# Performance work log

Measured on AMD Instinct MI355X. Metric: run time of the kernel, lower is better.

Reference implementation:

```python
import jax, jax.numpy as jnp
import numpy as np

NUM_HEADS = 12
WINDOW = (14, 14)


def gen_relative_position_index(ws):
    num_rel = (2 * ws[0] - 1) * (2 * ws[1] - 1) + 3
    coords = np.stack(np.meshgrid(np.arange(ws[0]), np.arange(ws[1]), indexing='ij'))
    cf = coords.reshape(2, -1)  # [2, Wh*Ww]
    rel = cf[:, :, None] - cf[:, None, :]  # [2, A, A]
    rel = rel.transpose(1, 2, 0).astype(np.int64)  # [A, A, 2]
    rel[..., 0] += ws[0] - 1
    rel[..., 1] += ws[1] - 1
    rel[..., 0] *= 2 * ws[1] - 1
    area = ws[0] * ws[1]
    idx = np.zeros((area + 1, area + 1), dtype=np.int64)
    idx[1:, 1:] = rel.sum(-1)
    idx[0, :] = num_rel - 3
    idx[:, 0] = num_rel - 2
    idx[0, 0] = num_rel - 1
    return idx


def setup_inputs() -> dict:
    key = jax.random.key(0)
    ks = jax.random.split(key, 7)
    B, N, C = 128, WINDOW[0] * WINDOW[1] + 1, 768
    num_rel = (2 * WINDOW[0] - 1) * (2 * WINDOW[1] - 1) + 3  # 732
    s = 0.02
    return {
        'x': jax.random.normal(ks[0], (B, N, C), jnp.float32),
        'qkv_w': jax.random.normal(ks[1], (3 * C, C), jnp.float32) * s,
        'q_bias': jax.random.normal(ks[2], (C,), jnp.float32) * s,
        'v_bias': jax.random.normal(ks[3], (C,), jnp.float32) * s,
        'rel_pos_table': jax.random.normal(ks[4], (num_rel, NUM_HEADS), jnp.float32) * s,
        'proj_w': jax.random.normal(ks[5], (C, C), jnp.float32) * s,
        'proj_b': jax.random.normal(ks[6], (C,), jnp.float32) * s,
        'rel_index': jnp.asarray(gen_relative_position_index(WINDOW)),
    }


def reference(x, qkv_w, q_bias, v_bias, rel_pos_table, proj_w, proj_b, rel_index):
    B, N, C = x.shape
    H = NUM_HEADS
    hd = C // H
    scale = hd ** -0.5
    # qkv projection with (q_bias, zeros, v_bias) composite bias
    bias = jnp.concatenate([q_bias, jnp.zeros_like(q_bias), v_bias])
    qkv = x @ qkv_w.T + bias  # [B, N, 3C]
    qkv = qkv.reshape(B, N, 3, H, hd).transpose(2, 0, 3, 1, 4)  # [3, B, H, N, hd]
    q, k, v = qkv[0], qkv[1], qkv[2]
    # gather relative position bias: [N, N, H] -> [H, N, N]
    rel_bias = rel_pos_table[rel_index.reshape(-1)].reshape(N, N, H).transpose(2, 0, 1)
    attn = jnp.einsum('bhnd,bhmd->bhnm', q * scale, k) + rel_bias[None]
    attn = jax.nn.softmax(attn, axis=-1)
    out = jnp.einsum('bhnm,bhmd->bhnd', attn, v)  # [B, H, N, hd]
    out = out.transpose(0, 2, 1, 3).reshape(B, N, C)
    return out @ proj_w.T + proj_b
```

## Files before the change

### kernel.cpp

```cpp
#include <hip/hip_runtime.h>

typedef unsigned short u16;
typedef __attribute__((ext_vector_type(8))) short short8;
typedef __attribute__((ext_vector_type(8))) __bf16 bf16x8;
typedef __attribute__((ext_vector_type(4))) float floatx4;

#define BATCH 128
#define SEQ 197
#define CH 768
#define NH 12
#define HD 64
#define MROWS (BATCH * SEQ)

__device__ __forceinline__ floatx4 mfma16(short8 a, short8 b, floatx4 c) {
  return __builtin_amdgcn_mfma_f32_16x16x32_bf16(
      __builtin_bit_cast(bf16x8, a), __builtin_bit_cast(bf16x8, b), c, 0, 0, 0);
}

__device__ __forceinline__ u16 f2bf(float f) {
  unsigned u = __builtin_bit_cast(unsigned, f);
  return (u16)((u + 0x7fffu + ((u >> 16) & 1u)) >> 16);
}

__device__ __forceinline__ void async16(const u16* g, u16* s) {
  __builtin_amdgcn_global_load_lds((const __attribute__((address_space(1))) void*)g,
                                   (__attribute__((address_space(3))) void*)s, 16, 0, 0);
}

__global__ __launch_bounds__(256) void preproc(const float4* __restrict__ x, ushort4* __restrict__ xo, int n0,
                                               const float4* __restrict__ w1, ushort4* __restrict__ w1o, int n1,
                                               const float4* __restrict__ w2, ushort4* __restrict__ w2o, int n2,
                                               const int* __restrict__ idx, const float* __restrict__ table,
                                               float* __restrict__ relb) {
  int i = blockIdx.x * 256 + threadIdx.x;
  const float4* in; ushort4* out; int j;
  if (i < n0) { in = x; out = xo; j = i; }
  else if (i < n0 + n1) { in = w1; out = w1o; j = i - n0; }
  else if (i < n0 + n1 + n2) { in = w2; out = w2o; j = i - n0 - n1; }
  else {
    int t = i - (n0 + n1 + n2);
    if (t < SEQ * SEQ) {
      int id = idx[t];
      const float* row = table + id * NH;
#pragma unroll
      for (int h = 0; h < NH; h++) relb[h * (SEQ * SEQ) + t] = row[h];
    }
    return;
  }
  float4 v = in[j];
  ushort4 o;
  o.x = f2bf(v.x); o.y = f2bf(v.y); o.z = f2bf(v.z); o.w = f2bf(v.w);
  out[j] = o;
}

__global__ __launch_bounds__(256, 2) void gemm_qkv(const u16* __restrict__ A,
                                                   const u16* __restrict__ W,
                                                   const float* __restrict__ qb,
                                                   const float* __restrict__ vb,
                                                   u16* __restrict__ q_buf,
                                                   u16* __restrict__ k_buf,
                                                   u16* __restrict__ v_buf) {
  __shared__ u16 As[128 * 32];
  __shared__ u16 Bs[256 * 32];
  int tid = threadIdx.x;
  int wave = tid >> 6, lane = tid & 63, quad = lane >> 4, c16 = lane & 15;
  int wm = wave >> 1, wn = wave & 1;
  int m0 = blockIdx.y * 128, n0 = blockIdx.x * 256;
  int lrow = lane >> 2;
  int lcol = (((lane & 3) ^ ((lane >> 3) & 3))) * 8;
  const u16* Ag0 = A + (size_t)(m0 + wave * 32 + lrow) * CH + lcol;
  const u16* Ag1 = Ag0 + (size_t)16 * CH;
  const u16* Bg0 = W + (size_t)(n0 + wave * 64 + lrow) * CH + lcol;
  const u16* Bg1 = Bg0 + (size_t)16 * CH;
  const u16* Bg2 = Bg0 + (size_t)32 * CH;
  const u16* Bg3 = Bg0 + (size_t)48 * CH;
  u16* AsW0 = As + (wave * 32) * 32;
  u16* AsW1 = As + (wave * 32 + 16) * 32;
  u16* BsW0 = Bs + (wave * 64) * 32;
  u16* BsW1 = Bs + (wave * 64 + 16) * 32;
  u16* BsW2 = Bs + (wave * 64 + 32) * 32;
  u16* BsW3 = Bs + (wave * 64 + 48) * 32;
  int fsl = (quad ^ ((c16 >> 1) & 3)) * 8;
  const u16* ArF = As + (wm * 64 + c16) * 32 + fsl;
  const u16* BrF = Bs + (wn * 128 + c16) * 32 + fsl;
  floatx4 acc[4][8] = {};
  for (int kk = 0; kk < CH; kk += 32) {
    __syncthreads();
    async16(Ag0 + kk, AsW0);
    async16(Ag1 + kk, AsW1);
    async16(Bg0 + kk, BsW0);
    async16(Bg1 + kk, BsW1);
    async16(Bg2 + kk, BsW2);
    async16(Bg3 + kk, BsW3);
    __syncthreads();
    short8 af[4], bfr[8];
#pragma unroll
    for (int i = 0; i < 4; i++) af[i] = *(const short8*)(ArF + i * 16 * 32);
#pragma unroll
    for (int j = 0; j < 8; j++) bfr[j] = *(const short8*)(BrF + j * 16 * 32);
#pragma unroll
    for (int i = 0; i < 4; i++)
#pragma unroll
      for (int j = 0; j < 8; j++) acc[i][j] = mfma16(af[i], bfr[j], acc[i][j]);
  }
#pragma unroll
  for (int j = 0; j < 8; j++) {
    int gcol = n0 + wn * 128 + j * 16 + c16;
    int t = gcol / CH;
    int rem = gcol - t * CH;
    int h = rem >> 6, d = rem & 63;
    float badd = (t == 0) ? qb[rem] : (t == 2 ? vb[rem] : 0.0f);
    u16* dst = (t == 0) ? q_buf : (t == 1 ? k_buf : v_buf);
#pragma unroll
    for (int i = 0; i < 4; i++) {
#pragma unroll
      for (int r = 0; r < 4; r++) {
        int grow = m0 + wm * 64 + i * 16 + quad * 4 + r;
        int bb = grow / SEQ;
        int n = grow - bb * SEQ;
        dst[(((size_t)bb * NH + h) * SEQ + n) * HD + d] = f2bf(acc[i][j][r] + badd);
      }
    }
  }
}

#define PS 232
#define VS 264

__global__ __launch_bounds__(256, 2) void attn(const u16* __restrict__ q_buf,
                                               const u16* __restrict__ k_buf,
                                               const u16* __restrict__ v_buf,
                                               const float* __restrict__ relb,
                                               u16* __restrict__ attn_out) {
  __shared__ u16 Vt[64 * VS];
  __shared__ u16 P[4 * 16 * PS];

  int h = blockIdx.x, b = blockIdx.y;
  int tid = threadIdx.x, wave = tid >> 6, lane = tid & 63, quad = lane >> 4, c16 = lane & 15;
  size_t bh = (size_t)b * NH + h;
  const u16* Q = q_buf + bh * SEQ * HD;
  const u16* Kp = k_buf + bh * SEQ * HD;
  const u16* Vp = v_buf + bh * SEQ * HD;
  const float* RB = relb + (size_t)h * (SEQ * SEQ);

  {
    int mrow = tid >> 3, dbase = (tid & 7) * 8;
#pragma unroll
    for (int i = 0; i < 7; i++) {
      int m = mrow + 32 * i;
      if (m < SEQ) {
        ushort4 v0 = *(const ushort4*)(Vp + m * HD + dbase);
        ushort4 v1 = *(const ushort4*)(Vp + m * HD + dbase + 4);
        Vt[(dbase + 0) * VS + m] = v0.x;
        Vt[(dbase + 1) * VS + m] = v0.y;
        Vt[(dbase + 2) * VS + m] = v0.z;
        Vt[(dbase + 3) * VS + m] = v0.w;
        Vt[(dbase + 4) * VS + m] = v1.x;
        Vt[(dbase + 5) * VS + m] = v1.y;
        Vt[(dbase + 6) * VS + m] = v1.z;
        Vt[(dbase + 7) * VS + m] = v1.w;
      } else {
#pragma unroll
        for (int dd = 0; dd < 8; dd++) Vt[(dbase + dd) * VS + m] = 0;
      }
    }
  }
  __syncthreads();

  u16* Pw = P + wave * 16 * PS;
  for (int rt = wave; rt < 13; rt += 4) {
    int q0 = rt * 16;
    int qr = min(q0 + c16, SEQ - 1);
    short8 qa0 = *(const short8*)(Q + qr * HD + quad * 8);
    short8 qa1 = *(const short8*)(Q + qr * HD + 32 + quad * 8);

    floatx4 sacc[13];
#pragma unroll
    for (int nt = 0; nt < 13; nt++) {
      int mc = min(nt * 16 + c16, SEQ - 1);
      floatx4 a = {0.f, 0.f, 0.f, 0.f};
      a = mfma16(qa0, *(const short8*)(Kp + mc * HD + quad * 8), a);
      a = mfma16(qa1, *(const short8*)(Kp + mc * HD + 32 + quad * 8), a);
      sacc[nt] = a;
    }

#pragma unroll
    for (int r = 0; r < 4; r++) {
      int rq = min(q0 + quad * 4 + r, SEQ - 1);
      const float* RBr = RB + (size_t)rq * SEQ;
      float mx = -1e30f;
#pragma unroll
      for (int nt = 0; nt < 13; nt++) {
        int m = nt * 16 + c16;
        float s = -1e30f;
        if (m < SEQ) s = sacc[nt][r] * 0.125f + RBr[m];
        sacc[nt][r] = s;
        mx = fmaxf(mx, s);
      }
      mx = fmaxf(mx, __shfl_xor(mx, 1));
      mx = fmaxf(mx, __shfl_xor(mx, 2));
      mx = fmaxf(mx, __shfl_xor(mx, 4));
      mx = fmaxf(mx, __shfl_xor(mx, 8));
      float sum = 0.f;
#pragma unroll
      for (int nt = 0; nt < 13; nt++) {
        float e = __expf(sacc[nt][r] - mx);
        sacc[nt][r] = e;
        sum += e;
      }
      sum += __shfl_xor(sum, 1);
      sum += __shfl_xor(sum, 2);
      sum += __shfl_xor(sum, 4);
      sum += __shfl_xor(sum, 8);
      float inv = 1.f / sum;
      int prow = (quad * 4 + r) * PS;
#pragma unroll
      for (int nt = 0; nt < 13; nt++)
        Pw[prow + nt * 16 + c16] = f2bf(sacc[nt][r] * inv);
      Pw[prow + 208 + c16] = 0;
    }

    floatx4 oacc[4] = {};
#pragma unroll
    for (int ks = 0; ks < 7; ks++) {
      short8 a = *(const short8*)(Pw + c16 * PS + ks * 32 + quad * 8);
#pragma unroll
      for (int dt = 0; dt < 4; dt++) {
        short8 bb = *(const short8*)(Vt + (dt * 16 + c16) * VS + ks * 32 + quad * 8);
        oacc[dt] = mfma16(a, bb, oacc[dt]);
      }
    }
#pragma unroll
    for (int dt = 0; dt < 4; dt++) {
      int d = dt * 16 + c16;
#pragma unroll
      for (int r = 0; r < 4; r++) {
        int grow = q0 + quad * 4 + r;
        if (grow < SEQ)
          attn_out[((size_t)b * SEQ + grow) * CH + h * HD + d] = f2bf(oacc[dt][r]);
      }
    }
  }
}

__global__ __launch_bounds__(256, 2) void gemm_proj(const u16* __restrict__ A,
                                                    const u16* __restrict__ W,
                                                    const float* __restrict__ bias,
                                                    float* __restrict__ out) {
  __shared__ u16 As[128 * 32];
  __shared__ u16 Bs[256 * 32];
  int tid = threadIdx.x;
  int wave = tid >> 6, lane = tid & 63, quad = lane >> 4, c16 = lane & 15;
  int wm = wave >> 1, wn = wave & 1;
  int m0 = blockIdx.y * 128, n0 = blockIdx.x * 256;
  int lrow = lane >> 2;
  int lcol = (((lane & 3) ^ ((lane >> 3) & 3))) * 8;
  const u16* Ag0 = A + (size_t)(m0 + wave * 32 + lrow) * CH + lcol;
  const u16* Ag1 = Ag0 + (size_t)16 * CH;
  const u16* Bg0 = W + (size_t)(n0 + wave * 64 + lrow) * CH + lcol;
  const u16* Bg1 = Bg0 + (size_t)16 * CH;
  const u16* Bg2 = Bg0 + (size_t)32 * CH;
  const u16* Bg3 = Bg0 + (size_t)48 * CH;
  u16* AsW0 = As + (wave * 32) * 32;
  u16* AsW1 = As + (wave * 32 + 16) * 32;
  u16* BsW0 = Bs + (wave * 64) * 32;
  u16* BsW1 = Bs + (wave * 64 + 16) * 32;
  u16* BsW2 = Bs + (wave * 64 + 32) * 32;
  u16* BsW3 = Bs + (wave * 64 + 48) * 32;
  int fsl = (quad ^ ((c16 >> 1) & 3)) * 8;
  const u16* ArF = As + (wm * 64 + c16) * 32 + fsl;
  const u16* BrF = Bs + (wn * 128 + c16) * 32 + fsl;
  floatx4 acc[4][8] = {};
  for (int kk = 0; kk < CH; kk += 32) {
    __syncthreads();
    async16(Ag0 + kk, AsW0);
    async16(Ag1 + kk, AsW1);
    async16(Bg0 + kk, BsW0);
    async16(Bg1 + kk, BsW1);
    async16(Bg2 + kk, BsW2);
    async16(Bg3 + kk, BsW3);
    __syncthreads();
    short8 af[4], bfr[8];
#pragma unroll
    for (int i = 0; i < 4; i++) af[i] = *(const short8*)(ArF + i * 16 * 32);
#pragma unroll
    for (int j = 0; j < 8; j++) bfr[j] = *(const short8*)(BrF + j * 16 * 32);
#pragma unroll
    for (int i = 0; i < 4; i++)
#pragma unroll
      for (int j = 0; j < 8; j++) acc[i][j] = mfma16(af[i], bfr[j], acc[i][j]);
  }
#pragma unroll
  for (int j = 0; j < 8; j++) {
    int gcol = n0 + wn * 128 + j * 16 + c16;
    float bj = bias[gcol];
#pragma unroll
    for (int i = 0; i < 4; i++)
#pragma unroll
      for (int r = 0; r < 4; r++) {
        int grow = m0 + wm * 64 + i * 16 + quad * 4 + r;
        out[(size_t)grow * CH + gcol] = acc[i][j][r] + bj;
      }
  }
}

extern "C" void kernel_launch(void* const* d_in, const int* in_sizes, int n_in,
                              void* d_out, int out_size, void* d_ws, size_t ws_size,
                              hipStream_t stream) {
  const float* x      = (const float*)d_in[0];
  const float* qkv_w  = (const float*)d_in[1];
  const float* q_bias = (const float*)d_in[2];
  const float* v_bias = (const float*)d_in[3];
  const float* table  = (const float*)d_in[4];
  const float* proj_w = (const float*)d_in[5];
  const float* proj_b = (const float*)d_in[6];
  const int*   rel_ix = (const int*)d_in[7];
  float* out = (float*)d_out;

  char* ws = (char*)d_ws;
  size_t off = 0;
  u16* x_bf  = (u16*)(ws + off); off += (size_t)MROWS * CH * 2;
  u16* wq_bf = (u16*)(ws + off); off += (size_t)3 * CH * CH * 2;
  u16* wp_bf = (u16*)(ws + off); off += (size_t)CH * CH * 2;
  u16* q_buf = (u16*)(ws + off); off += (size_t)MROWS * CH * 2;
  u16* k_buf = (u16*)(ws + off); off += (size_t)MROWS * CH * 2;
  u16* v_buf = (u16*)(ws + off); off += (size_t)MROWS * CH * 2;
  u16* ao_bf = (u16*)(ws + off); off += (size_t)MROWS * CH * 2;
  float* relb = (float*)(ws + off);

  int n0 = MROWS * CH / 4;
  int n1 = 3 * CH * CH / 4;
  int n2 = CH * CH / 4;
  int ntot = n0 + n1 + n2 + SEQ * SEQ;
  preproc<<<(ntot + 255) / 256, 256, 0, stream>>>(
      (const float4*)x, (ushort4*)x_bf, n0,
      (const float4*)qkv_w, (ushort4*)wq_bf, n1,
      (const float4*)proj_w, (ushort4*)wp_bf, n2,
      rel_ix, table, relb);
  gemm_qkv<<<dim3(9, 197), 256, 0, stream>>>(x_bf, wq_bf, q_bias, v_bias, q_buf, k_buf, v_buf);
  attn<<<dim3(NH, BATCH), 256, 0, stream>>>(q_buf, k_buf, v_buf, relb, ao_bf);
  gemm_proj<<<dim3(3, 197), 256, 0, stream>>>(ao_bf, wp_bf, proj_b, out);
}
```

Before: 419.7 us.

## Double-buffer LDS in QKV and proj GEMMs and remap blocks per XCD

Result: faster. 402.6 us (-4.1%).

```diff
diff --git a/kernel.cpp b/kernel.cpp
--- a/kernel.cpp
+++ b/kernel.cpp
@@ -60,12 +60,21 @@
                                                    u16* __restrict__ q_buf,
                                                    u16* __restrict__ k_buf,
                                                    u16* __restrict__ v_buf) {
-  __shared__ u16 As[128 * 32];
-  __shared__ u16 Bs[256 * 32];
+  __shared__ u16 S[2][(128 + 256) * 32];
+  const int BUF = (128 + 256) * 32;
+  const int BOFF = 128 * 32;
   int tid = threadIdx.x;
   int wave = tid >> 6, lane = tid & 63, quad = lane >> 4, c16 = lane & 15;
   int wm = wave >> 1, wn = wave & 1;
-  int m0 = blockIdx.y * 128, n0 = blockIdx.x * 256;
+
+  int nwg = gridDim.x;
+  int orig = blockIdx.x;
+  int xcd = orig & 7, pos = orig >> 3;
+  int qq = nwg >> 3, rr = nwg & 7;
+  int lid = (xcd < rr ? xcd * (qq + 1) : rr * (qq + 1) + (xcd - rr) * qq) + pos;
+  int mblk = lid / 9, nblk = lid - mblk * 9;
+  int m0 = mblk * 128, n0 = nblk * 256;
+
   int lrow = lane >> 2;
   int lcol = (((lane & 3) ^ ((lane >> 3) & 3))) * 8;
   const u16* Ag0 = A + (size_t)(m0 + wave * 32 + lrow) * CH + lcol;
@@ -74,35 +83,67 @@
   const u16* Bg1 = Bg0 + (size_t)16 * CH;
   const u16* Bg2 = Bg0 + (size_t)32 * CH;
   const u16* Bg3 = Bg0 + (size_t)48 * CH;
-  u16* AsW0 = As + (wave * 32) * 32;
-  u16* AsW1 = As + (wave * 32 + 16) * 32;
-  u16* BsW0 = Bs + (wave * 64) * 32;
-  u16* BsW1 = Bs + (wave * 64 + 16) * 32;
-  u16* BsW2 = Bs + (wave * 64 + 32) * 32;
-  u16* BsW3 = Bs + (wave * 64 + 48) * 32;
+  int aw0 = (wave * 32) * 32;
+  int aw1 = (wave * 32 + 16) * 32;
+  int bw0 = BOFF + (wave * 64) * 32;
+  int bw1 = BOFF + (wave * 64 + 16) * 32;
+  int bw2 = BOFF + (wave * 64 + 32) * 32;
+  int bw3 = BOFF + (wave * 64 + 48) * 32;
   int fsl = (quad ^ ((c16 >> 1) & 3)) * 8;
-  const u16* ArF = As + (wm * 64 + c16) * 32 + fsl;
-  const u16* BrF = Bs + (wn * 128 + c16) * 32 + fsl;
+  int aro = (wm * 64 + c16) * 32 + fsl;
+  int bro = BOFF + (wn * 128 + c16) * 32 + fsl;
+
   floatx4 acc[4][8] = {};
-  for (int kk = 0; kk < CH; kk += 32) {
-    __syncthreads();
-    async16(Ag0 + kk, AsW0);
-    async16(Ag1 + kk, AsW1);
-    async16(Bg0 + kk, BsW0);
-    async16(Bg1 + kk, BsW1);
-    async16(Bg2 + kk, BsW2);
-    async16(Bg3 + kk, BsW3);
-    __syncthreads();
+  u16* sbase = &S[0][0];
+
+  async16(Ag0, sbase + aw0);
+  async16(Ag1, sbase + aw1);
+  async16(Bg0, sbase + bw0);
+  async16(Bg1, sbase + bw1);
+  async16(Bg2, sbase + bw2);
+  async16(Bg3, sbase + bw3);
+  asm volatile("s_waitcnt vmcnt(0)" ::: "memory");
+  __builtin_amdgcn_s_barrier();
+  asm volatile("" ::: "memory");
+
+  int cur = 0;
+  for (int kt = 1; kt < CH / 32; ++kt) {
+    int kk = kt * 32;
+    u16* sn = sbase + (cur ^ 1) * BUF;
+    async16(Ag0 + kk, sn + aw0);
+    async16(Ag1 + kk, sn + aw1);
+    async16(Bg0 + kk, sn + bw0);
+    async16(Bg1 + kk, sn + bw1);
+    async16(Bg2 + kk, sn + bw2);
+    async16(Bg3 + kk, sn + bw3);
+    const u16* sc = sbase + cur * BUF;
     short8 af[4], bfr[8];
 #pragma unroll
-    for (int i = 0; i < 4; i++) af[i] = *(const short8*)(ArF + i * 16 * 32);
-#pragma unroll
-    for (int j = 0; j < 8; j++) bfr[j] = *(const short8*)(BrF + j * 16 * 32);
+    for (int i = 0; i < 4; i++) af[i] = *(const short8*)(sc + aro + i * 16 * 32);
+#pragma unroll
+    for (int j = 0; j < 8; j++) bfr[j] = *(const short8*)(sc + bro + j * 16 * 32);
 #pragma unroll
     for (int i = 0; i < 4; i++)
 #pragma unroll
       for (int j = 0; j < 8; j++) acc[i][j] = mfma16(af[i], bfr[j], acc[i][j]);
-  }
+    asm volatile("s_waitcnt vmcnt(0)" ::: "memory");
+    __builtin_amdgcn_s_barrier();
+    asm volatile("" ::: "memory");
+    cur ^= 1;
+  }
+  {
+    const u16* sc = sbase + cur * BUF;
+    short8 af[4], bfr[8];
+#pragma unroll
+    for (int i = 0; i < 4; i++) af[i] = *(const short8*)(sc + aro + i * 16 * 32);
+#pragma unroll
+    for (int j = 0; j < 8; j++) bfr[j] = *(const short8*)(sc + bro + j * 16 * 32);
+#pragma unroll
+    for (int i = 0; i < 4; i++)
+#pragma unroll
+      for (int j = 0; j < 8; j++) acc[i][j] = mfma16(af[i], bfr[j], acc[i][j]);
+  }
+
 #pragma unroll
   for (int j = 0; j < 8; j++) {
     int gcol = n0 + wn * 128 + j * 16 + c16;
@@ -247,12 +288,21 @@
                                                     const u16* __restrict__ W,
                                                     const float* __restrict__ bias,
                                                     float* __restrict__ out) {
-  __shared__ u16 As[128 * 32];
-  __shared__ u16 Bs[256 * 32];
+  __shared__ u16 S[2][(128 + 256) * 32];
+  const int BUF = (128 + 256) * 32;
+  const int BOFF = 128 * 32;
   int tid = threadIdx.x;
   int wave = tid >> 6, lane = tid & 63, quad = lane >> 4, c16 = lane & 15;
   int wm = wave >> 1, wn = wave & 1;
-  int m0 = blockIdx.y * 128, n0 = blockIdx.x * 256;
+
+  int nwg = gridDim.x;
+  int orig = blockIdx.x;
+  int xcd = orig & 7, pos = orig >> 3;
+  int qq = nwg >> 3, rr = nwg & 7;
+  int lid = (xcd < rr ? xcd * (qq + 1) : rr * (qq + 1) + (xcd - rr) * qq) + pos;
+  int mblk = lid / 3, nblk = lid - mblk * 3;
+  int m0 = mblk * 128, n0 = nblk * 256;
+
   int lrow = lane >> 2;
   int lcol = (((lane & 3) ^ ((lane >> 3) & 3))) * 8;
   const u16* Ag0 = A + (size_t)(m0 + wave * 32 + lrow) * CH + lcol;
@@ -261,35 +311,67 @@
   const u16* Bg1 = Bg0 + (size_t)16 * CH;
   const u16* Bg2 = Bg0 + (size_t)32 * CH;
   const u16* Bg3 = Bg0 + (size_t)48 * CH;
-  u16* AsW0 = As + (wave * 32) * 32;
-  u16* AsW1 = As + (wave * 32 + 16) * 32;
-  u16* BsW0 = Bs + (wave * 64) * 32;
-  u16* BsW1 = Bs + (wave * 64 + 16) * 32;
-  u16* BsW2 = Bs + (wave * 64 + 32) * 32;
-  u16* BsW3 = Bs + (wave * 64 + 48) * 32;
+  int aw0 = (wave * 32) * 32;
+  int aw1 = (wave * 32 + 16) * 32;
+  int bw0 = BOFF + (wave * 64) * 32;
+  int bw1 = BOFF + (wave * 64 + 16) * 32;
+  int bw2 = BOFF + (wave * 64 + 32) * 32;
+  int bw3 = BOFF + (wave * 64 + 48) * 32;
   int fsl = (quad ^ ((c16 >> 1) & 3)) * 8;
-  const u16* ArF = As + (wm * 64 + c16) * 32 + fsl;
-  const u16* BrF = Bs + (wn * 128 + c16) * 32 + fsl;
+  int aro = (wm * 64 + c16) * 32 + fsl;
+  int bro = BOFF + (wn * 128 + c16) * 32 + fsl;
+
   floatx4 acc[4][8] = {};
-  for (int kk = 0; kk < CH; kk += 32) {
-    __syncthreads();
-    async16(Ag0 + kk, AsW0);
-    async16(Ag1 + kk, AsW1);
-    async16(Bg0 + kk, BsW0);
-    async16(Bg1 + kk, BsW1);
-    async16(Bg2 + kk, BsW2);
-    async16(Bg3 + kk, BsW3);
-    __syncthreads();
+  u16* sbase = &S[0][0];
+
+  async16(Ag0, sbase + aw0);
+  async16(Ag1, sbase + aw1);
+  async16(Bg0, sbase + bw0);
+  async16(Bg1, sbase + bw1);
+  async16(Bg2, sbase + bw2);
+  async16(Bg3, sbase + bw3);
+  asm volatile("s_waitcnt vmcnt(0)" ::: "memory");
+  __builtin_amdgcn_s_barrier();
+  asm volatile("" ::: "memory");
+
+  int cur = 0;
+  for (int kt = 1; kt < CH / 32; ++kt) {
+    int kk = kt * 32;
+    u16* sn = sbase + (cur ^ 1) * BUF;
+    async16(Ag0 + kk, sn + aw0);
+    async16(Ag1 + kk, sn + aw1);
+    async16(Bg0 + kk, sn + bw0);
+    async16(Bg1 + kk, sn + bw1);
+    async16(Bg2 + kk, sn + bw2);
+    async16(Bg3 + kk, sn + bw3);
+    const u16* sc = sbase + cur * BUF;
     short8 af[4], bfr[8];
 #pragma unroll
-    for (int i = 0; i < 4; i++) af[i] = *(const short8*)(ArF + i * 16 * 32);
-#pragma unroll
-    for (int j = 0; j < 8; j++) bfr[j] = *(const short8*)(BrF + j * 16 * 32);
+    for (int i = 0; i < 4; i++) af[i] = *(const short8*)(sc + aro + i * 16 * 32);
+#pragma unroll
+    for (int j = 0; j < 8; j++) bfr[j] = *(const short8*)(sc + bro + j * 16 * 32);
 #pragma unroll
     for (int i = 0; i < 4; i++)
 #pragma unroll
       for (int j = 0; j < 8; j++) acc[i][j] = mfma16(af[i], bfr[j], acc[i][j]);
-  }
+    asm volatile("s_waitcnt vmcnt(0)" ::: "memory");
+    __builtin_amdgcn_s_barrier();
+    asm volatile("" ::: "memory");
+    cur ^= 1;
+  }
+  {
+    const u16* sc = sbase + cur * BUF;
+    short8 af[4], bfr[8];
+#pragma unroll
+    for (int i = 0; i < 4; i++) af[i] = *(const short8*)(sc + aro + i * 16 * 32);
+#pragma unroll
+    for (int j = 0; j < 8; j++) bfr[j] = *(const short8*)(sc + bro + j * 16 * 32);
+#pragma unroll
+    for (int i = 0; i < 4; i++)
+#pragma unroll
+      for (int j = 0; j < 8; j++) acc[i][j] = mfma16(af[i], bfr[j], acc[i][j]);
+  }
+
 #pragma unroll
   for (int j = 0; j < 8; j++) {
     int gcol = n0 + wn * 128 + j * 16 + c16;
@@ -337,7 +419,7 @@
       (const float4*)qkv_w, (ushort4*)wq_bf, n1,
       (const float4*)proj_w, (ushort4*)wp_bf, n2,
       rel_ix, table, relb);
-  gemm_qkv<<<dim3(9, 197), 256, 0, stream>>>(x_bf, wq_bf, q_bias, v_bias, q_buf, k_buf, v_buf);
+  gemm_qkv<<<dim3(197 * 9), 256, 0, stream>>>(x_bf, wq_bf, q_bias, v_bias, q_buf, k_buf, v_buf);
   attn<<<dim3(NH, BATCH), 256, 0, stream>>>(q_buf, k_buf, v_buf, relb, ao_bf);
-  gemm_proj<<<dim3(3, 197), 256, 0, stream>>>(ao_bf, wp_bf, proj_b, out);
-}
+  gemm_proj<<<dim3(197 * 3), 256, 0, stream>>>(ao_bf, wp_bf, proj_b, out);
+}
```

## Rewrite QKV/proj GEMMs with 256x256x64 double-buffered tiles and XCD-aware block mapping

Applied to the files above, without the earlier changes.

Measured after the change: 508.6 us. 21.2% more time.

```diff
diff --git a/kernel.cpp b/kernel.cpp
--- a/kernel.cpp
+++ b/kernel.cpp
@@ -11,6 +11,11 @@
 #define NH 12
 #define HD 64
 #define MROWS (BATCH * SEQ)
+#define MPAD 25344
+
+#define TM 256
+#define TN 256
+#define TK 64
 
 __device__ __forceinline__ floatx4 mfma16(short8 a, short8 b, floatx4 c) {
   return __builtin_amdgcn_mfma_f32_16x16x32_bf16(
@@ -44,6 +49,12 @@
       const float* row = table + id * NH;
 #pragma unroll
       for (int h = 0; h < NH; h++) relb[h * (SEQ * SEQ) + t] = row[h];
+    } else {
+      int p = t - SEQ * SEQ;
+      if (p < (MPAD - MROWS) * CH / 4) {
+        ushort4 z = {0, 0, 0, 0};
+        xo[n0 + p] = z;
+      }
     }
     return;
   }
@@ -53,72 +64,140 @@
   out[j] = o;
 }
 
-__global__ __launch_bounds__(256, 2) void gemm_qkv(const u16* __restrict__ A,
+
+#define STAGE8(Sb_, kk_)                                                       \
+  do {                                                                         \
+    u16* sa_ = (Sb_) + wave * 8 * TK;                                          \
+    u16* sb_ = (Sb_) + TM * TK + wave * 8 * TK;                                \
+    const u16* ga_ = Agp + (kk_);                                              \
+    const u16* gb_ = Bgp + (kk_);                                              \
+    _Pragma("unroll")                                                          \
+    for (int r_ = 0; r_ < 4; r_++)                                             \
+      async16(ga_ + (size_t)r_ * 64 * CH, sa_ + r_ * 64 * TK);                 \
+    _Pragma("unroll")                                                          \
+    for (int r_ = 0; r_ < 4; r_++)                                             \
+      async16(gb_ + (size_t)r_ * 64 * CH, sb_ + r_ * 64 * TK);                 \
+  } while (0)
+
+#define QUAD(Sb_, qr_, qc_)                                                    \
+  do {                                                                         \
+    const u16* sa_ = (Sb_);                                                    \
+    const u16* sb_ = (Sb_) + TM * TK;                                          \
+    int pof0_ = ((quad) ^ (c16 & 7)) * 8;                                      \
+    int pof1_ = ((4 + quad) ^ (c16 & 7)) * 8;                                  \
+    short8 av_[4][2], bv_[2][2];                                               \
+    _Pragma("unroll")                                                          \
+    for (int i_ = 0; i_ < 4; i_++) {                                           \
+      int R_ = wm * 128 + ((qr_) * 4 + i_) * 16 + c16;                         \
+      av_[i_][0] = *(const short8*)(sa_ + R_ * TK + pof0_);                    \
+      av_[i_][1] = *(const short8*)(sa_ + R_ * TK + pof1_);                    \
+    }                                                                          \
+    _Pragma("unroll")                                                          \
+    for (int j_ = 0; j_ < 2; j_++) {                                           \
+      int R_ = wn * 64 + ((qc_) * 2 + j_) * 16 + c16;                          \
+      bv_[j_][0] = *(const short8*)(sb_ + R_ * TK + pof0_);                    \
+      bv_[j_][1] = *(const short8*)(sb_ + R_ * TK + pof1_);                    \
+    }                                                                          \
+    __builtin_amdgcn_s_setprio(1);                                             \
+    _Pragma("unroll")                                                          \
+    for (int i_ = 0; i_ < 4; i_++)                                             \
+      _Pragma("unroll")                                                        \
+      for (int j_ = 0; j_ < 2; j_++) {                                         \
+        acc[(qr_) * 4 + i_][(qc_) * 2 + j_] =                                  \
+            mfma16(av_[i_][0], bv_[j_][0], acc[(qr_) * 4 + i_][(qc_) * 2 + j_]); \
+        acc[(qr_) * 4 + i_][(qc_) * 2 + j_] =                                  \
+            mfma16(av_[i_][1], bv_[j_][1], acc[(qr_) * 4 + i_][(qc_) * 2 + j_]); \
+      }                                                                        \
+    __builtin_amdgcn_s_setprio(0);                                             \
+  } while (0)
+
+#define PBAR()                                                                 \
+  do {                                                                         \
+    asm volatile("" ::: "memory");                                             \
+    __builtin_amdgcn_s_barrier();                                              \
+    asm volatile("" ::: "memory");                                             \
+  } while (0)
+
+#define GEMM_PRE_AND_LOOP(Amat_, Wmat_, NBLK_)                                 \
+  __shared__ u16 S[2][2 * TM * TK];                                \
+  int tid = threadIdx.x;                                                       \
+  int wave = tid >> 6, lane = tid & 63, quad = lane >> 4, c16 = lane & 15;     \
+  int wm = wave >> 2, wn = wave & 3;                                           \
+  int nwg = gridDim.x;                                                         \
+  int orig = blockIdx.x;                                                       \
+  int xcd = orig & 7, pos = orig >> 3;                                         \
+  int qq = nwg >> 3, rr = nwg & 7;                                             \
+  int lid = (xcd < rr ? xcd * (qq + 1) : rr * (qq + 1) + (xcd - rr) * qq) + pos; \
+  int mblk = lid / (NBLK_), nblk = lid - mblk * (NBLK_);                       \
+  int m0 = mblk * TM, n0 = nblk * TN;                                          \
+  int lr = lane >> 3;                                                          \
+  int lg = (lane & 7) ^ lr;                                                    \
+  const u16* Agp = (Amat_) + (size_t)(m0 + wave * 8 + lr) * CH + lg * 8;       \
+  const u16* Bgp = (Wmat_) + (size_t)(n0 + wave * 8 + lr) * CH + lg * 8;       \
+  floatx4 acc[8][4] = {};                                                      \
+  STAGE8(&S[0][0], 0);                                                         \
+  asm volatile("s_waitcnt vmcnt(0)" ::: "memory");                             \
+  __builtin_amdgcn_s_barrier();                                                \
+  asm volatile("" ::: "memory");                                               \
+  for (int kt = 0; kt < CH / TK; ++kt) {                                       \
+    int cb = kt & 1;                                                           \
+    if (kt < CH / TK - 1) STAGE8(&S[cb ^ 1][0], (kt + 1) * TK);                \
+    QUAD(&S[cb][0], 0, 0); PBAR();                                             \
+    QUAD(&S[cb][0], 0, 1); PBAR();                                             \
+    QUAD(&S[cb][0], 1, 0); PBAR();                                             \
+    QUAD(&S[cb][0], 1, 1);                                                     \
+    if (kt < CH / TK - 1) asm volatile("s_waitcnt vmcnt(0)" ::: "memory");     \
+    PBAR();                                                                    \
+  }
+
+__global__ __launch_bounds__(512, 2) void gemm_qkv(const u16* __restrict__ A,
                                                    const u16* __restrict__ W,
                                                    const float* __restrict__ qb,
                                                    const float* __restrict__ vb,
                                                    u16* __restrict__ q_buf,
                                                    u16* __restrict__ k_buf,
                                                    u16* __restrict__ v_buf) {
-  __shared__ u16 As[128 * 32];
-  __shared__ u16 Bs[256 * 32];
-  int tid = threadIdx.x;
-  int wave = tid >> 6, lane = tid & 63, quad = lane >> 4, c16 = lane & 15;
-  int wm = wave >> 1, wn = wave & 1;
-  int m0 = blockIdx.y * 128, n0 = blockIdx.x * 256;
-  int lrow = lane >> 2;
-  int lcol = (((lane & 3) ^ ((lane >> 3) & 3))) * 8;
-  const u16* Ag0 = A + (size_t)(m0 + wave * 32 + lrow) * CH + lcol;
-  const u16* Ag1 = Ag0 + (size_t)16 * CH;
-  const u16* Bg0 = W + (size_t)(n0 + wave * 64 + lrow) * CH + lcol;
-  const u16* Bg1 = Bg0 + (size_t)16 * CH;
-  const u16* Bg2 = Bg0 + (size_t)32 * CH;
-  const u16* Bg3 = Bg0 + (size_t)48 * CH;
-  u16* AsW0 = As + (wave * 32) * 32;
-  u16* AsW1 = As + (wave * 32 + 16) * 32;
-  u16* BsW0 = Bs + (wave * 64) * 32;
-  u16* BsW1 = Bs + (wave * 64 + 16) * 32;
-  u16* BsW2 = Bs + (wave * 64 + 32) * 32;
-  u16* BsW3 = Bs + (wave * 64 + 48) * 32;
-  int fsl = (quad ^ ((c16 >> 1) & 3)) * 8;
-  const u16* ArF = As + (wm * 64 + c16) * 32 + fsl;
-  const u16* BrF = Bs + (wn * 128 + c16) * 32 + fsl;
-  floatx4 acc[4][8] = {};
-  for (int kk = 0; kk < CH; kk += 32) {
-    __syncthreads();
-    async16(Ag0 + kk, AsW0);
-    async16(Ag1 + kk, AsW1);
-    async16(Bg0 + kk, BsW0);
-    async16(Bg1 + kk, BsW1);
-    async16(Bg2 + kk, BsW2);
-    async16(Bg3 + kk, BsW3);
-    __syncthreads();
-    short8 af[4], bfr[8];
-#pragma unroll
-    for (int i = 0; i < 4; i++) af[i] = *(const short8*)(ArF + i * 16 * 32);
-#pragma unroll
-    for (int j = 0; j < 8; j++) bfr[j] = *(const short8*)(BrF + j * 16 * 32);
-#pragma unroll
-    for (int i = 0; i < 4; i++)
-#pragma unroll
-      for (int j = 0; j < 8; j++) acc[i][j] = mfma16(af[i], bfr[j], acc[i][j]);
-  }
-#pragma unroll
-  for (int j = 0; j < 8; j++) {
-    int gcol = n0 + wn * 128 + j * 16 + c16;
+  GEMM_PRE_AND_LOOP(A, W, 9)
+
+#pragma unroll
+  for (int j = 0; j < 4; j++) {
+    int gcol = n0 + wn * 64 + j * 16 + c16;
     int t = gcol / CH;
     int rem = gcol - t * CH;
     int h = rem >> 6, d = rem & 63;
     float badd = (t == 0) ? qb[rem] : (t == 2 ? vb[rem] : 0.0f);
     u16* dst = (t == 0) ? q_buf : (t == 1 ? k_buf : v_buf);
 #pragma unroll
-    for (int i = 0; i < 4; i++) {
+    for (int i = 0; i < 8; i++) {
 #pragma unroll
       for (int r = 0; r < 4; r++) {
-        int grow = m0 + wm * 64 + i * 16 + quad * 4 + r;
-        int bb = grow / SEQ;
-        int n = grow - bb * SEQ;
-        dst[(((size_t)bb * NH + h) * SEQ + n) * HD + d] = f2bf(acc[i][j][r] + badd);
+        int grow = m0 + wm * 128 + i * 16 + quad * 4 + r;
+        if (grow < MROWS) {
+          int bb = grow / SEQ;
+          int n = grow - bb * SEQ;
+          dst[(((size_t)bb * NH + h) * SEQ + n) * HD + d] = f2bf(acc[i][j][r] + badd);
+        }
+      }
+    }
+  }
+}
+
+__global__ __launch_bounds__(512, 2) void gemm_proj(const u16* __restrict__ A,
+                                                    const u16* __restrict__ W,
+                                                    const float* __restrict__ bias,
+                                                    float* __restrict__ out) {
+  GEMM_PRE_AND_LOOP(A, W, 3)
+
+#pragma unroll
+  for (int j = 0; j < 4; j++) {
+    int gcol = n0 + wn * 64 + j * 16 + c16;
+    float bj = bias[gcol];
+#pragma unroll
+    for (int i = 0; i < 8; i++) {
+#pragma unroll
+      for (int r = 0; r < 4; r++) {
+        int grow = m0 + wm * 128 + i * 16 + quad * 4 + r;
+        if (grow < MROWS) out[(size_t)grow * CH + gcol] = acc[i][j][r] + bj;
       }
     }
   }
@@ -175,6 +254,7 @@
     short8 qa1 = *(const short8*)(Q + qr * HD + 32 + quad * 8);
 
     floatx4 sacc[13];
+    __builtin_amdgcn_s_setprio(1);
 #pragma unroll
     for (int nt = 0; nt < 13; nt++) {
       int mc = min(nt * 16 + c16, SEQ - 1);
@@ -183,6 +263,7 @@
       a = mfma16(qa1, *(const short8*)(Kp + mc * HD + 32 + quad * 8), a);
       sacc[nt] = a;
     }
+    __builtin_amdgcn_s_setprio(0);
 
 #pragma unroll
     for (int r = 0; r < 4; r++) {
@@ -221,6 +302,7 @@
     }
 
     floatx4 oacc[4] = {};
+    __builtin_amdgcn_s_setprio(1);
 #pragma unroll
     for (int ks = 0; ks < 7; ks++) {
       short8 a = *(const short8*)(Pw + c16 * PS + ks * 32 + quad * 8);
@@ -230,6 +312,7 @@
         oacc[dt] = mfma16(a, bb, oacc[dt]);
       }
     }
+    __builtin_amdgcn_s_setprio(0);
 #pragma unroll
     for (int dt = 0; dt < 4; dt++) {
       int d = dt * 16 + c16;
@@ -240,67 +323,6 @@
           attn_out[((size_t)b * SEQ + grow) * CH + h * HD + d] = f2bf(oacc[dt][r]);
       }
     }
-  }
-}
-
-__global__ __launch_bounds__(256, 2) void gemm_proj(const u16* __restrict__ A,
-                                                    const u16* __restrict__ W,
-                                                    const float* __restrict__ bias,
-                                                    float* __restrict__ out) {
-  __shared__ u16 As[128 * 32];
-  __shared__ u16 Bs[256 * 32];
-  int tid = threadIdx.x;
-  int wave = tid >> 6, lane = tid & 63, quad = lane >> 4, c16 = lane & 15;
-  int wm = wave >> 1, wn = wave & 1;
-  int m0 = blockIdx.y * 128, n0 = blockIdx.x * 256;
-  int lrow = lane >> 2;
-  int lcol = (((lane & 3) ^ ((lane >> 3) & 3))) * 8;
-  const u16* Ag0 = A + (size_t)(m0 + wave * 32 + lrow) * CH + lcol;
-  const u16* Ag1 = Ag0 + (size_t)16 * CH;
-  const u16* Bg0 = W + (size_t)(n0 + wave * 64 + lrow) * CH + lcol;
-  const u16* Bg1 = Bg0 + (size_t)16 * CH;
-  const u16* Bg2 = Bg0 + (size_t)32 * CH;
-  const u16* Bg3 = Bg0 + (size_t)48 * CH;
-  u16* AsW0 = As + (wave * 32) * 32;
-  u16* AsW1 = As + (wave * 32 + 16) * 32;
-  u16* BsW0 = Bs + (wave * 64) * 32;
-  u16* BsW1 = Bs + (wave * 64 + 16) * 32;
-  u16* BsW2 = Bs + (wave * 64 + 32) * 32;
-  u16* BsW3 = Bs + (wave * 64 + 48) * 32;
-  int fsl = (quad ^ ((c16 >> 1) & 3)) * 8;
-  const u16* ArF = As + (wm * 64 + c16) * 32 + fsl;
-  const u16* BrF = Bs + (wn * 128 + c16) * 32 + fsl;
-  floatx4 acc[4][8] = {};
-  for (int kk = 0; kk < CH; kk += 32) {
-    __syncthreads();
-    async16(Ag0 + kk, AsW0);
-    async16(Ag1 + kk, AsW1);
-    async16(Bg0 + kk, BsW0);
-    async16(Bg1 + kk, BsW1);
-    async16(Bg2 + kk, BsW2);
-    async16(Bg3 + kk, BsW3);
-    __syncthreads();
-    short8 af[4], bfr[8];
-#pragma unroll
-    for (int i = 0; i < 4; i++) af[i] = *(const short8*)(ArF + i * 16 * 32);
-#pragma unroll
-    for (int j = 0; j < 8; j++) bfr[j] = *(const short8*)(BrF + j * 16 * 32);
-#pragma unroll
-    for (int i = 0; i < 4; i++)
-#pragma unroll
-      for (int j = 0; j < 8; j++) acc[i][j] = mfma16(af[i], bfr[j], acc[i][j]);
-  }
-#pragma unroll
-  for (int j = 0; j < 8; j++) {
-    int gcol = n0 + wn * 128 + j * 16 + c16;
-    float bj = bias[gcol];
-#pragma unroll
-    for (int i = 0; i < 4; i++)
-#pragma unroll
-      for (int r = 0; r < 4; r++) {
-        int grow = m0 + wm * 64 + i * 16 + quad * 4 + r;
-        out[(size_t)grow * CH + gcol] = acc[i][j][r] + bj;
-      }
   }
 }
 
@@ -319,25 +341,26 @@
 
   char* ws = (char*)d_ws;
   size_t off = 0;
-  u16* x_bf  = (u16*)(ws + off); off += (size_t)MROWS * CH * 2;
+  u16* x_bf  = (u16*)(ws + off); off += (size_t)MPAD * CH * 2;
   u16* wq_bf = (u16*)(ws + off); off += (size_t)3 * CH * CH * 2;
   u16* wp_bf = (u16*)(ws + off); off += (size_t)CH * CH * 2;
   u16* q_buf = (u16*)(ws + off); off += (size_t)MROWS * CH * 2;
   u16* k_buf = (u16*)(ws + off); off += (size_t)MROWS * CH * 2;
   u16* v_buf = (u16*)(ws + off); off += (size_t)MROWS * CH * 2;
-  u16* ao_bf = (u16*)(ws + off); off += (size_t)MROWS * CH * 2;
+  u16* ao_bf = (u16*)(ws + off); off += (size_t)MPAD * CH * 2;
   float* relb = (float*)(ws + off);
 
   int n0 = MROWS * CH / 4;
   int n1 = 3 * CH * CH / 4;
   int n2 = CH * CH / 4;
-  int ntot = n0 + n1 + n2 + SEQ * SEQ;
+  int npad = (MPAD - MROWS) * CH / 4;
+  int ntot = n0 + n1 + n2 + SEQ * SEQ + npad;
   preproc<<<(ntot + 255) / 256, 256, 0, stream>>>(
       (const float4*)x, (ushort4*)x_bf, n0,
       (const float4*)qkv_w, (ushort4*)wq_bf, n1,
       (const float4*)proj_w, (ushort4*)wp_bf, n2,
       rel_ix, table, relb);
-  gemm_qkv<<<dim3(9, 197), 256, 0, stream>>>(x_bf, wq_bf, q_bias, v_bias, q_buf, k_buf, v_buf);
+  gemm_qkv<<<dim3(99 * 9), 512, 0, stream>>>(x_bf, wq_bf, q_bias, v_bias, q_buf, k_buf, v_buf);
   attn<<<dim3(NH, BATCH), 256, 0, stream>>>(q_buf, k_buf, v_buf, relb, ao_bf);
-  gemm_proj<<<dim3(3, 197), 256, 0, stream>>>(ao_bf, wp_bf, proj_b, out);
-}
+  gemm_proj<<<dim3(99 * 3), 512, 0, stream>>>(ao_bf, wp_bf, proj_b, out);
+}
```
